# Kernel optimization log

Hardware: AMD Instinct MI355X
Metric: run time of the kernel (lower is better)

Reference implementation:

```python
import jax, jax.numpy as jnp
import numpy as np
import math

HEADS = 8
DIM_KEY = 64
WINDOW = 128
DIM = 512
NUM_REL_POS_FEATURES = 512  # = HEADS*DIM_KEY; %4==0 and %6!=0 -> exp + central_mask features
W_WIDTH, W_FRAC = 8, 4
X_WIDTH, X_FRAC = 8, 4


def quantize(x, width, frac_width):
    # MASE integer_quantizer: fixed-point round+clamp (STE in bwd, identity here).
    scale = 2.0 ** frac_width
    lo = -(2.0 ** (width - 1))
    hi = 2.0 ** (width - 1) - 1.0
    q = jnp.clip(jnp.round(x * scale), lo, hi) / scale
    return x + jax.lax.stop_gradient(q - x)


def get_positional_embed(window, feature_size):
    # distances in [-(W-1), W-1]
    d = jnp.arange(-(window - 1), window, dtype=jnp.float32)  # [2W-1]
    nb = feature_size // 4  # 2 feature fns * 2 components
    ad = jnp.abs(d)[:, None]
    # exponential features
    max_range = math.log(window) / math.log(2.0)
    half_life = 2.0 ** jnp.linspace(3.0, max_range, nb)
    e = jnp.exp(-math.log(2.0) / half_life[None, :] * ad)  # [2W-1, nb]
    # central mask features (2**128 overflows to inf in f32, matching torch)
    cw = 2.0 ** jnp.arange(1, nb + 1, dtype=jnp.float32) - 1.0
    c = (cw[None, :] > ad).astype(jnp.float32)  # [2W-1, nb]
    emb = jnp.concatenate([e, c], axis=-1)  # [2W-1, 2*nb]
    return jnp.concatenate([emb, jnp.sign(d)[:, None] * emb], axis=-1)  # [2W-1, 4*nb]


def relative_shift_swin(x):
    # x: [b, h, w, t1, t2] with t2 = 2*t1 - 1 -> [b, h, w, t1, t1]
    b, h, w, t1, t2 = x.shape
    x = jnp.concatenate([jnp.zeros_like(x[..., :1]), x], axis=-1)  # pad -> t2+1 = 2*t1
    t2p = t2 + 1
    x = x.reshape(b, h, w, t2p, t1)[:, :, :, 1:, :]
    x = x.reshape(b, h, w, t1, t2p - 1)
    return x[..., :(t2p + 1) // 2]


def setup_inputs() -> dict:
    key = jax.random.key(0)
    ks = jax.random.split(key, 7)
    b, n = 4, 8192
    hd = HEADS * DIM_KEY
    return {
        "x": jax.random.normal(ks[0], (b, n, DIM), dtype=jnp.float32),
        "w_qkv": jax.random.normal(ks[1], (hd * 3, DIM), dtype=jnp.float32) * 0.02,
        "w_out": jax.random.normal(ks[2], (DIM, hd), dtype=jnp.float32) * 0.02,
        "b_out": jnp.zeros((DIM,), dtype=jnp.float32),
        "w_rel": jax.random.normal(ks[3], (hd, NUM_REL_POS_FEATURES), dtype=jnp.float32) * 0.02,
        "rel_content_bias": jax.random.normal(ks[4], (1, HEADS, 1, 1, DIM_KEY), dtype=jnp.float32),
        "rel_pos_bias": jax.random.normal(ks[5], (1, HEADS, 1, 1, DIM_KEY), dtype=jnp.float32),
    }


def reference(x, w_qkv, w_out, b_out, w_rel, rel_content_bias, rel_pos_bias):
    b, n, c = x.shape
    w = n // WINDOW  # n divisible by window -> no padding path
    xq = quantize(x, X_WIDTH, X_FRAC)
    wq = quantize(w_qkv, W_WIDTH, W_FRAC)
    wo = quantize(w_out, W_WIDTH, W_FRAC)

    qkv = xq @ wq.T  # [b, n, 3*h*d], last dim laid out as (h, d, k)
    qkv = qkv.reshape(b, n, HEADS, DIM_KEY, 3)
    q = qkv[..., 0].transpose(0, 2, 1, 3)  # [b, h, n, d]
    k = qkv[..., 1].transpose(0, 2, 1, 3)
    v = qkv[..., 2].transpose(0, 2, 1, 3)

    qw = q.reshape(b, HEADS, w, WINDOW, DIM_KEY)
    kw = k.reshape(b, HEADS, w, WINDOW, DIM_KEY)
    vw = v.reshape(b, HEADS, w, WINDOW, DIM_KEY)

    positions = get_positional_embed(WINDOW, NUM_REL_POS_FEATURES)  # [2W-1, F]
    rel_k = positions @ w_rel.T  # [2W-1, h*d]  (rel_pos_embedding weight is NOT quantized)
    rel_k = rel_k.reshape(2 * WINDOW - 1, HEADS, DIM_KEY).transpose(1, 0, 2)  # [h, 2W-1, d]

    scale = DIM_KEY ** -0.5
    content_attn = jnp.einsum('bhwqd,bhwkd->bhwqk', qw + rel_content_bias, kw) * scale
    # NB: positional logits are intentionally unscaled, as in the source.
    rel_logits = jnp.einsum('bhwqd,hkd->bhwqk', qw + rel_pos_bias, rel_k)  # [b,h,w,W,2W-1]
    position_attn = relative_shift_swin(rel_logits)  # [b,h,w,W,W]

    attn = jax.nn.softmax(content_attn + position_attn, axis=-1)
    out = jnp.einsum('bhwqk,bhwkd->bhwqd', attn, vw)  # [b,h,w,W,d]
    out = out.transpose(0, 2, 3, 1, 4).reshape(b, w, WINDOW, HEADS * DIM_KEY)
    out = out @ wo.T + b_out  # [b, w, W, dim]
    return out.reshape(b, n, -1)
```

## Files before the change

kernel.cpp:

```cpp
#include <hip/hip_runtime.h>

typedef unsigned short u16;
typedef unsigned int u32;
typedef __attribute__((ext_vector_type(8))) __bf16 bf16x8;
typedef __attribute__((ext_vector_type(4))) float f32x4;
typedef __attribute__((ext_vector_type(8))) unsigned short u16x8;
typedef __attribute__((ext_vector_type(4))) unsigned short u16x4;

#define GLL(gp, lp) __builtin_amdgcn_global_load_lds((const __attribute__((address_space(1))) void*)(gp), (__attribute__((address_space(3))) void*)(lp), 16, 0, 0)

__device__ __forceinline__ u16 f2bf(float f) {
  u32 u = __float_as_uint(f);
  u += 0x7FFFu + ((u >> 16) & 1u);
  return (u16)(u >> 16);
}
__device__ __forceinline__ float bf2f(u16 u) { return __uint_as_float(((u32)u) << 16); }
__device__ __forceinline__ float qz(float v) {
  float r = rintf(v * 16.0f);
  r = fminf(127.0f, fmaxf(-128.0f, r));
  return r * 0.0625f;
}
__device__ __forceinline__ f32x4 mfma16(bf16x8 a, bf16x8 b, f32x4 c) {
  return __builtin_amdgcn_mfma_f32_16x16x32_bf16(a, b, c, 0, 0, 0);
}

__global__ __launch_bounds__(256) void k_quant(const float* __restrict__ x,
                                               const float* __restrict__ wqkv,
                                               const float* __restrict__ wout,
                                               u16* __restrict__ xq,
                                               u16* __restrict__ wq,
                                               u16* __restrict__ wo) {
  const int X4 = 4194304;
  const int W4 = 196608;
  const int O4 = 65536;
  int stride = gridDim.x * blockDim.x;
  for (int i = blockIdx.x * blockDim.x + threadIdx.x; i < X4 + W4 + O4; i += stride) {
    const float4* s; u16* d; int j;
    if (i < X4)            { s = (const float4*)x;    d = xq; j = i; }
    else if (i < X4 + W4)  { s = (const float4*)wqkv; d = wq; j = i - X4; }
    else                   { s = (const float4*)wout; d = wo; j = i - X4 - W4; }
    float4 v = s[j];
    u16x4 o;
    o.x = f2bf(qz(v.x)); o.y = f2bf(qz(v.y)); o.z = f2bf(qz(v.z)); o.w = f2bf(qz(v.w));
    *(u16x4*)(d + (size_t)j * 4) = o;
  }
}

__global__ __launch_bounds__(128) void k_relk(const float* __restrict__ w_rel,
                                              const float* __restrict__ pb,
                                              u16* __restrict__ relk,
                                              float* __restrict__ pbR) {
  int r = blockIdx.x;
  int cseg = blockIdx.y;
  int tid = threadIdx.x;
  int c = cseg * 128 + tid;
  if (r == 255) {
    relk[((size_t)(c >> 6) * 256 + 255) * 64 + (c & 63)] = 0;
    if ((tid & 63) == 0) pbR[(c >> 6) * 256 + 255] = 0.f;
    return;
  }
  __shared__ float pos[512];
  float dd = (float)(r - 127);
  float ad = fabsf(dd);
  float sg = (dd > 0.f) ? 1.f : ((dd < 0.f) ? -1.f : 0.f);
  for (int f = tid; f < 512; f += 128) {
    int base = f & 255;
    float feat;
    if (base < 128) {
      float hl = exp2f(3.0f + (float)base * (4.0f / 127.0f));
      feat = expf((-0.6931471805599453f / hl) * ad);
    } else {
      float cw = exp2f((float)(base - 128 + 1)) - 1.0f;
      feat = (cw > ad) ? 1.0f : 0.0f;
    }
    if (f >= 256) feat *= sg;
    pos[f] = feat;
  }
  __syncthreads();
  const float4* wr4 = (const float4*)(w_rel + (size_t)c * 512);
  float acc = 0.f;
  #pragma unroll 4
  for (int f4 = 0; f4 < 128; f4++) {
    float4 w4 = wr4[f4];
    int f = f4 * 4;
    acc += pos[f] * w4.x + pos[f + 1] * w4.y + pos[f + 2] * w4.z + pos[f + 3] * w4.w;
  }
  relk[((size_t)(c >> 6) * 256 + r) * 64 + (c & 63)] = f2bf(acc);
  float contrib = acc * pb[c];
  #pragma unroll
  for (int off = 1; off < 64; off <<= 1) contrib += __shfl_xor(contrib, off, 64);
  if ((tid & 63) == 0) pbR[(c >> 6) * 256 + r] = contrib;
}

__global__ __launch_bounds__(256) void k_gemm_qkv(const u16* __restrict__ Aq,
                                                  const u16* __restrict__ Bq,
                                                  u16* __restrict__ Qo,
                                                  u16* __restrict__ Ko,
                                                  u16* __restrict__ Vo) {
  __shared__ u16 As[128 * 32];
  __shared__ u16 Bs[128 * 32];
  int tid = threadIdx.x;
  int bid = blockIdx.x;
  int swz = (bid & 7) * (gridDim.x >> 3) + (bid >> 3);
  int m0 = (swz / 12) * 128, n0 = (swz % 12) * 128;
  int wid = tid >> 6, lane = tid & 63, g = lane >> 4, r16 = lane & 15;
  int wm = wid >> 1, wn = wid & 1;
  f32x4 acc[4][4];
  #pragma unroll
  for (int i = 0; i < 4; i++)
    #pragma unroll
    for (int j = 0; j < 4; j++) acc[i][j] = (f32x4){0.f, 0.f, 0.f, 0.f};
  const u16* Ab = Aq + (size_t)m0 * 512;
  const u16* Bb = Bq + (size_t)n0 * 512;
  char* AsB = (char*)As + wid * 1024;
  char* BsB = (char*)Bs + wid * 1024;
  for (int k0 = 0; k0 < 512; k0 += 32) {
    __syncthreads();
    GLL(Ab + (size_t)(tid >> 2) * 512 + k0 + (tid & 3) * 8, AsB);
    GLL(Ab + (size_t)((tid >> 2) + 64) * 512 + k0 + (tid & 3) * 8, AsB + 4096);
    GLL(Bb + (size_t)(tid >> 2) * 512 + k0 + (tid & 3) * 8, BsB);
    GLL(Bb + (size_t)((tid >> 2) + 64) * 512 + k0 + (tid & 3) * 8, BsB + 4096);
    __syncthreads();
    bf16x8 a[4], b[4];
    #pragma unroll
    for (int mt = 0; mt < 4; mt++)
      a[mt] = *(const bf16x8*)(As + (wm * 64 + mt * 16 + r16) * 32 + g * 8);
    #pragma unroll
    for (int nt = 0; nt < 4; nt++)
      b[nt] = *(const bf16x8*)(Bs + (wn * 64 + nt * 16 + r16) * 32 + g * 8);
    #pragma unroll
    for (int mt = 0; mt < 4; mt++)
      #pragma unroll
      for (int nt = 0; nt < 4; nt++) acc[mt][nt] = mfma16(a[mt], b[nt], acc[mt][nt]);
  }
  #pragma unroll
  for (int nt = 0; nt < 4; nt++) {
    int col = n0 + wn * 64 + nt * 16 + r16;
    int h = col / 192;
    int rem = col - h * 192;
    int dd = rem / 3;
    int comp = rem - dd * 3;
    u16* dst = (comp == 0) ? Qo : (comp == 1 ? Ko : Vo);
    #pragma unroll
    for (int mt = 0; mt < 4; mt++) {
      int mbase = m0 + wm * 64 + mt * 16 + 4 * g;
      #pragma unroll
      for (int rr = 0; rr < 4; rr++) {
        int m = mbase + rr;
        int bb = m >> 13, nn = m & 8191;
        dst[((size_t)(bb * 8 + h) * 8192 + nn) * 64 + dd] = f2bf(acc[mt][nt][rr]);
      }
    }
  }
}

__global__ __launch_bounds__(512) void k_attn(const u16* __restrict__ Q,
                                              const u16* __restrict__ K,
                                              const u16* __restrict__ V,
                                              const u16* __restrict__ relk,
                                              const float* __restrict__ pbR,
                                              const float* __restrict__ cb,
                                              u16* __restrict__ attout) {
  int bid = blockIdx.x;
  int bb = bid >> 9;
  int h = (bid >> 6) & 7;
  int w = bid & 63;
  int tid = threadIdx.x;
  int s = tid >> 6;
  int lane = tid & 63, g = lane >> 4, r16 = lane & 15;
  const int n0 = w * 128;
  const u16* Qh = Q + ((size_t)(bb * 8 + h) * 8192 + n0) * 64;
  const u16* Kh = K + ((size_t)(bb * 8 + h) * 8192 + n0) * 64;
  const u16* Vh = V + ((size_t)(bb * 8 + h) * 8192 + n0) * 64;
  const u16* Rh = relk + (size_t)h * 256 * 64;
  const float* pbRh = pbR + h * 256;

  __shared__ u16 VT[64 * 128];
  __shared__ u16 Pst[8 * 16 * 128];
  __shared__ float cbK[128];

  {
    int rv = tid >> 2, c0 = (tid & 3) << 4;
    const u16* src = Vh + rv * 64 + c0;
    u16x8 v0 = *(const u16x8*)src;
    u16x8 v1 = *(const u16x8*)(src + 8);
    int chunk = rv >> 3, sub = rv & 7;
    #pragma unroll
    for (int j = 0; j < 8; j++) {
      int dv = c0 + j;
      VT[dv * 128 + ((chunk ^ (dv & 7)) << 3) + sub] = v0[j];
    }
    #pragma unroll
    for (int j = 0; j < 8; j++) {
      int dv = c0 + 8 + j;
      VT[dv * 128 + ((chunk ^ (dv & 7)) << 3) + sub] = v1[j];
    }
  }
  if (tid < 128) {
    const u16* kr = Kh + tid * 64;
    const float* cbh = cb + h * 64;
    float a = 0.f;
    #pragma unroll 8
    for (int d = 0; d < 64; d++) a += cbh[d] * bf2f(kr[d]);
    cbK[tid] = a;
  }

  const u16* qptr = Qh + ((s << 4) + r16) * 64 + (g << 3);
  bf16x8 qa0 = *(const bf16x8*)qptr;
  bf16x8 qa1 = *(const bf16x8*)(qptr + 32);

  f32x4 sc[8];
  #pragma unroll
  for (int kt = 0; kt < 8; kt++) {
    const u16* kp = Kh + ((kt << 4) + r16) * 64 + (g << 3);
    bf16x8 b0 = *(const bf16x8*)kp;
    bf16x8 b1 = *(const bf16x8*)(kp + 32);
    f32x4 c = {0.f, 0.f, 0.f, 0.f};
    c = mfma16(qa0, b0, c);
    sc[kt] = mfma16(qa1, b1, c);
  }
  f32x4 rl[9];
  #pragma unroll
  for (int t = 0; t < 9; t++) {
    int ct = 7 - s + t;
    const u16* rp = Rh + ((ct << 4) + r16) * 64 + (g << 3);
    bf16x8 b0 = *(const bf16x8*)rp;
    bf16x8 b1 = *(const bf16x8*)(rp + 32);
    f32x4 c = {0.f, 0.f, 0.f, 0.f};
    c = mfma16(qa0, b0, c);
    c = mfma16(qa1, b1, c);
    float pv = pbRh[(ct << 4) + r16];
    c[0] += pv; c[1] += pv; c[2] += pv; c[3] += pv;
    rl[t] = c;
  }
  __syncthreads();

  #pragma unroll
  for (int kt = 0; kt < 8; kt++) {
    float cbk = cbK[(kt << 4) + r16];
    #pragma unroll
    for (int rr = 0; rr < 4; rr++) {
      int qq = 4 * g + rr;
      int loc = 15 + r16 - qq;
      int srcl = (g << 4) | (loc & 15);
      float vlo = __shfl(rl[kt][rr], srcl, 64);
      float vhi = __shfl(rl[kt + 1][rr], srcl, 64);
      float pos = (loc < 16) ? vlo : vhi;
      sc[kt][rr] = (sc[kt][rr] + cbk) * 0.125f + pos;
    }
  }
  float inv[4];
  #pragma unroll
  for (int rr = 0; rr < 4; rr++) {
    float m = sc[0][rr];
    #pragma unroll
    for (int kt = 1; kt < 8; kt++) m = fmaxf(m, sc[kt][rr]);
    #pragma unroll
    for (int off = 1; off < 16; off <<= 1) m = fmaxf(m, __shfl_xor(m, off, 64));
    float sum = 0.f;
    #pragma unroll
    for (int kt = 0; kt < 8; kt++) {
      float p = expf(sc[kt][rr] - m);
      sc[kt][rr] = p;
      sum += p;
    }
    #pragma unroll
    for (int off = 1; off < 16; off <<= 1) sum += __shfl_xor(sum, off, 64);
    inv[rr] = 1.0f / sum;
  }
  u16* Pw = Pst + s * (16 * 128);
  #pragma unroll
  for (int kt = 0; kt < 8; kt++) {
    #pragma unroll
    for (int rr = 0; rr < 4; rr++) {
      int qq = 4 * g + rr;
      int k = (kt << 4) + r16;
      Pw[qq * 128 + ((((k >> 3)) ^ (qq & 7)) << 3) + (k & 7)] = f2bf(sc[kt][rr]);
    }
  }
  f32x4 o[4];
  #pragma unroll
  for (int dvt = 0; dvt < 4; dvt++) o[dvt] = (f32x4){0.f, 0.f, 0.f, 0.f};
  #pragma unroll
  for (int koff = 0; koff < 128; koff += 32) {
    int ach = (koff >> 3) + g;
    bf16x8 a = *(const bf16x8*)(Pw + r16 * 128 + ((ach ^ (r16 & 7)) << 3));
    #pragma unroll
    for (int dvt = 0; dvt < 4; dvt++) {
      int dv = dvt * 16 + r16;
      bf16x8 bv = *(const bf16x8*)(VT + dv * 128 + ((ach ^ (dv & 7)) << 3));
      o[dvt] = mfma16(a, bv, o[dvt]);
    }
  }
  #pragma unroll
  for (int dvt = 0; dvt < 4; dvt++) {
    #pragma unroll
    for (int rr = 0; rr < 4; rr++) {
      int qq = 4 * g + rr;
      int nrow = n0 + (s << 4) + qq;
      int colo = h * 64 + dvt * 16 + r16;
      attout[((size_t)bb * 8192 + nrow) * 512 + colo] = f2bf(o[dvt][rr] * inv[rr]);
    }
  }
}

__global__ __launch_bounds__(256) void k_gemm_out(const u16* __restrict__ Aq,
                                                  const u16* __restrict__ Bq,
                                                  const float* __restrict__ bias,
                                                  float* __restrict__ out) {
  __shared__ u16 As[128 * 32];
  __shared__ u16 Bs[128 * 32];
  int tid = threadIdx.x;
  int bid = blockIdx.x;
  int swz = (bid & 7) * (gridDim.x >> 3) + (bid >> 3);
  int m0 = (swz >> 2) * 128, n0 = (swz & 3) * 128;
  int wid = tid >> 6, lane = tid & 63, g = lane >> 4, r16 = lane & 15;
  int wm = wid >> 1, wn = wid & 1;
  f32x4 acc[4][4];
  #pragma unroll
  for (int i = 0; i < 4; i++)
    #pragma unroll
    for (int j = 0; j < 4; j++) acc[i][j] = (f32x4){0.f, 0.f, 0.f, 0.f};
  const u16* Ab = Aq + (size_t)m0 * 512;
  const u16* Bb = Bq + (size_t)n0 * 512;
  char* AsB = (char*)As + wid * 1024;
  char* BsB = (char*)Bs + wid * 1024;
  for (int k0 = 0; k0 < 512; k0 += 32) {
    __syncthreads();
    GLL(Ab + (size_t)(tid >> 2) * 512 + k0 + (tid & 3) * 8, AsB);
    GLL(Ab + (size_t)((tid >> 2) + 64) * 512 + k0 + (tid & 3) * 8, AsB + 4096);
    GLL(Bb + (size_t)(tid >> 2) * 512 + k0 + (tid & 3) * 8, BsB);
    GLL(Bb + (size_t)((tid >> 2) + 64) * 512 + k0 + (tid & 3) * 8, BsB + 4096);
    __syncthreads();
    bf16x8 a[4], b[4];
    #pragma unroll
    for (int mt = 0; mt < 4; mt++)
      a[mt] = *(const bf16x8*)(As + (wm * 64 + mt * 16 + r16) * 32 + g * 8);
    #pragma unroll
    for (int nt = 0; nt < 4; nt++)
      b[nt] = *(const bf16x8*)(Bs + (wn * 64 + nt * 16 + r16) * 32 + g * 8);
    #pragma unroll
    for (int mt = 0; mt < 4; mt++)
      #pragma unroll
      for (int nt = 0; nt < 4; nt++) acc[mt][nt] = mfma16(a[mt], b[nt], acc[mt][nt]);
  }
  #pragma unroll
  for (int nt = 0; nt < 4; nt++) {
    int col = n0 + wn * 64 + nt * 16 + r16;
    float bv = bias[col];
    #pragma unroll
    for (int mt = 0; mt < 4; mt++) {
      int mbase = m0 + wm * 64 + mt * 16 + 4 * g;
      #pragma unroll
      for (int rr = 0; rr < 4; rr++) {
        int m = mbase + rr;
        out[(size_t)m * 512 + col] = acc[mt][nt][rr] + bv;
      }
    }
  }
}

extern "C" void kernel_launch(void* const* d_in, const int* in_sizes, int n_in,
                              void* d_out, int out_size, void* d_ws, size_t ws_size,
                              hipStream_t stream) {
  const float* x     = (const float*)d_in[0];
  const float* w_qkv = (const float*)d_in[1];
  const float* w_out = (const float*)d_in[2];
  const float* b_out = (const float*)d_in[3];
  const float* w_rel = (const float*)d_in[4];
  const float* cb    = (const float*)d_in[5];
  const float* pb    = (const float*)d_in[6];
  float* out = (float*)d_out;

  char* p = (char*)d_ws;
  u16* xq   = (u16*)p; p += (size_t)32768 * 512 * 2;
  u16* wq   = (u16*)p; p += (size_t)1536 * 512 * 2;
  u16* wo   = (u16*)p; p += (size_t)512 * 512 * 2;
  u16* relk = (u16*)p; p += (size_t)8 * 256 * 64 * 2;
  float* pbR = (float*)p; p += (size_t)8 * 256 * 4;
  u16* Qb   = (u16*)p; p += (size_t)4 * 8 * 8192 * 64 * 2;
  u16* Kb   = (u16*)p; p += (size_t)4 * 8 * 8192 * 64 * 2;
  u16* Vb   = (u16*)p; p += (size_t)4 * 8 * 8192 * 64 * 2;
  u16* att  = (u16*)p; p += (size_t)32768 * 512 * 2;

  hipLaunchKernelGGL(k_quant, dim3(2048), dim3(256), 0, stream, x, w_qkv, w_out, xq, wq, wo);
  hipLaunchKernelGGL(k_relk, dim3(256, 4), dim3(128), 0, stream, w_rel, pb, relk, pbR);
  hipLaunchKernelGGL(k_gemm_qkv, dim3(3072), dim3(256), 0, stream, xq, wq, Qb, Kb, Vb);
  hipLaunchKernelGGL(k_attn, dim3(2048), dim3(512), 0, stream, Qb, Kb, Vb, relk, pbR, cb, att);
  hipLaunchKernelGGL(k_gemm_out, dim3(1024), dim3(256), 0, stream, att, wo, b_out, out);
}
```

Before: 411.8 us.

## Permute QKV weight rows, XOR-swizzle GEMM LDS tiles, vectorize K-bias dot

The quantization kernel now writes the QKV weight with its rows permuted into [component][head][dim] order. Each QKV GEMM output column then maps to Q/K/V by a shift and mask instead of division by 192 and 3, and writes to each destination are contiguous across lanes. Both GEMMs apply an XOR swizzle to the column chunk used when staging tiles into LDS and when reading them back, to reduce LDS bank conflicts on the fragment reads. The content-bias dot product in attention loads K rows as 8-wide vectors. The permuted weight layout must stay consistent between the producer and consumer kernels.

```diff
diff --git a/kernel.cpp b/kernel.cpp
--- a/kernel.cpp
+++ b/kernel.cpp
@@ -35,14 +35,26 @@
   const int O4 = 65536;
   int stride = gridDim.x * blockDim.x;
   for (int i = blockIdx.x * blockDim.x + threadIdx.x; i < X4 + W4 + O4; i += stride) {
-    const float4* s; u16* d; int j;
-    if (i < X4)            { s = (const float4*)x;    d = xq; j = i; }
-    else if (i < X4 + W4)  { s = (const float4*)wqkv; d = wq; j = i - X4; }
-    else                   { s = (const float4*)wout; d = wo; j = i - X4 - W4; }
-    float4 v = s[j];
+    const float4* s; u16* d; int jl, jd;
+    if (i < X4) {
+      s = (const float4*)x; d = xq; jl = i; jd = i;
+    } else if (i < X4 + W4) {
+      s = (const float4*)wqkv; d = wq;
+      jl = i - X4;
+      int rs = jl >> 7;
+      int jc = jl & 127;
+      int h = rs / 192;
+      int rem = rs - h * 192;
+      int dd = rem / 3;
+      int comp = rem - dd * 3;
+      jd = (comp * 512 + h * 64 + dd) * 128 + jc;
+    } else {
+      s = (const float4*)wout; d = wo; jl = i - X4 - W4; jd = jl;
+    }
+    float4 v = s[jl];
     u16x4 o;
     o.x = f2bf(qz(v.x)); o.y = f2bf(qz(v.y)); o.z = f2bf(qz(v.z)); o.w = f2bf(qz(v.w));
-    *(u16x4*)(d + (size_t)j * 4) = o;
+    *(u16x4*)(d + (size_t)jd * 4) = o;
   }
 }
 
@@ -114,20 +126,23 @@
   const u16* Bb = Bq + (size_t)n0 * 512;
   char* AsB = (char*)As + wid * 1024;
   char* BsB = (char*)Bs + wid * 1024;
+  int srow = tid >> 2;
+  int scol = ((tid & 3) ^ ((tid >> 3) & 3)) * 8;
+  int gs = (g ^ ((r16 >> 1) & 3)) * 8;
   for (int k0 = 0; k0 < 512; k0 += 32) {
     __syncthreads();
-    GLL(Ab + (size_t)(tid >> 2) * 512 + k0 + (tid & 3) * 8, AsB);
-    GLL(Ab + (size_t)((tid >> 2) + 64) * 512 + k0 + (tid & 3) * 8, AsB + 4096);
-    GLL(Bb + (size_t)(tid >> 2) * 512 + k0 + (tid & 3) * 8, BsB);
-    GLL(Bb + (size_t)((tid >> 2) + 64) * 512 + k0 + (tid & 3) * 8, BsB + 4096);
+    GLL(Ab + (size_t)srow * 512 + k0 + scol, AsB);
+    GLL(Ab + (size_t)(srow + 64) * 512 + k0 + scol, AsB + 4096);
+    GLL(Bb + (size_t)srow * 512 + k0 + scol, BsB);
+    GLL(Bb + (size_t)(srow + 64) * 512 + k0 + scol, BsB + 4096);
     __syncthreads();
     bf16x8 a[4], b[4];
     #pragma unroll
     for (int mt = 0; mt < 4; mt++)
-      a[mt] = *(const bf16x8*)(As + (wm * 64 + mt * 16 + r16) * 32 + g * 8);
+      a[mt] = *(const bf16x8*)(As + (wm * 64 + mt * 16 + r16) * 32 + gs);
     #pragma unroll
     for (int nt = 0; nt < 4; nt++)
-      b[nt] = *(const bf16x8*)(Bs + (wn * 64 + nt * 16 + r16) * 32 + g * 8);
+      b[nt] = *(const bf16x8*)(Bs + (wn * 64 + nt * 16 + r16) * 32 + gs);
     #pragma unroll
     for (int mt = 0; mt < 4; mt++)
       #pragma unroll
@@ -135,12 +150,11 @@
   }
   #pragma unroll
   for (int nt = 0; nt < 4; nt++) {
-    int col = n0 + wn * 64 + nt * 16 + r16;
-    int h = col / 192;
-    int rem = col - h * 192;
-    int dd = rem / 3;
-    int comp = rem - dd * 3;
+    int colc = n0 + wn * 64 + nt * 16 + r16;
+    int comp = colc >> 9;
+    int hd = colc & 511;
     u16* dst = (comp == 0) ? Qo : (comp == 1 ? Ko : Vo);
+    u16* dstp = dst + (size_t)(hd >> 6) * 524288 + (hd & 63);
     #pragma unroll
     for (int mt = 0; mt < 4; mt++) {
       int mbase = m0 + wm * 64 + mt * 16 + 4 * g;
@@ -148,7 +162,7 @@
       for (int rr = 0; rr < 4; rr++) {
         int m = mbase + rr;
         int bb = m >> 13, nn = m & 8191;
-        dst[((size_t)(bb * 8 + h) * 8192 + nn) * 64 + dd] = f2bf(acc[mt][nt][rr]);
+        dstp[(size_t)bb * 4194304 + (size_t)nn * 64] = f2bf(acc[mt][nt][rr]);
       }
     }
   }
@@ -197,11 +211,15 @@
     }
   }
   if (tid < 128) {
-    const u16* kr = Kh + tid * 64;
+    const u16x8* kr8 = (const u16x8*)(Kh + tid * 64);
     const float* cbh = cb + h * 64;
     float a = 0.f;
-    #pragma unroll 8
-    for (int d = 0; d < 64; d++) a += cbh[d] * bf2f(kr[d]);
+    #pragma unroll
+    for (int d8 = 0; d8 < 8; d8++) {
+      u16x8 kv = kr8[d8];
+      #pragma unroll
+      for (int j = 0; j < 8; j++) a += cbh[d8 * 8 + j] * bf2f(kv[j]);
+    }
     cbK[tid] = a;
   }
 
@@ -325,20 +343,23 @@
   const u16* Bb = Bq + (size_t)n0 * 512;
   char* AsB = (char*)As + wid * 1024;
   char* BsB = (char*)Bs + wid * 1024;
+  int srow = tid >> 2;
+  int scol = ((tid & 3) ^ ((tid >> 3) & 3)) * 8;
+  int gs = (g ^ ((r16 >> 1) & 3)) * 8;
   for (int k0 = 0; k0 < 512; k0 += 32) {
     __syncthreads();
-    GLL(Ab + (size_t)(tid >> 2) * 512 + k0 + (tid & 3) * 8, AsB);
-    GLL(Ab + (size_t)((tid >> 2) + 64) * 512 + k0 + (tid & 3) * 8, AsB + 4096);
-    GLL(Bb + (size_t)(tid >> 2) * 512 + k0 + (tid & 3) * 8, BsB);
-    GLL(Bb + (size_t)((tid >> 2) + 64) * 512 + k0 + (tid & 3) * 8, BsB + 4096);
+    GLL(Ab + (size_t)srow * 512 + k0 + scol, AsB);
+    GLL(Ab + (size_t)(srow + 64) * 512 + k0 + scol, AsB + 4096);
+    GLL(Bb + (size_t)srow * 512 + k0 + scol, BsB);
+    GLL(Bb + (size_t)(srow + 64) * 512 + k0 + scol, BsB + 4096);
     __syncthreads();
     bf16x8 a[4], b[4];
     #pragma unroll
     for (int mt = 0; mt < 4; mt++)
-      a[mt] = *(const bf16x8*)(As + (wm * 64 + mt * 16 + r16) * 32 + g * 8);
+      a[mt] = *(const bf16x8*)(As + (wm * 64 + mt * 16 + r16) * 32 + gs);
     #pragma unroll
     for (int nt = 0; nt < 4; nt++)
-      b[nt] = *(const bf16x8*)(Bs + (wn * 64 + nt * 16 + r16) * 32 + g * 8);
+      b[nt] = *(const bf16x8*)(Bs + (wn * 64 + nt * 16 + r16) * 32 + gs);
     #pragma unroll
     for (int mt = 0; mt < 4; mt++)
       #pragma unroll
```

Result: faster. 359.5 us (-12.7%).
